# Kernel tuning notes

Hardware: AMD Instinct MI355X
Metric: run time of the kernel (lower is better)

Reference implementation:

```python
import jax, jax.numpy as jnp
import numpy as np

HEADS = 8
DIM_HEAD = 64
DIM = 512
LN_EPS = 1e-5


def rotate_half(t):
    shp = t.shape
    t = t.reshape(*shp[:-1], -1, 2)
    t1, t2 = t[..., 0], t[..., 1]
    return jnp.stack((-t2, t1), axis=-1).reshape(shp)


def apply_rope(freqs, t):
    # freqs: (b,1,n,dh) broadcast against t: (b,h,n,dh); rot_dim == dh so no pass-through
    return t * jnp.cos(freqs) + rotate_half(t) * jnp.sin(freqs)


def layer_norm(x, g, b, eps=LN_EPS):
    mu = jnp.mean(x, axis=-1, keepdims=True)
    var = jnp.var(x, axis=-1, keepdims=True)
    return (x - mu) * jax.lax.rsqrt(var + eps) * g + b


def setup_inputs() -> dict:
    key = jax.random.key(0)
    ks = jax.random.split(key, 8)
    n, b = 2048, 4
    inner = HEADS * DIM_HEAD
    inp = {
        "x": jax.random.normal(ks[0], (n, b, DIM), dtype=jnp.float32),
        "rot_pos_emb": jax.random.uniform(ks[1], (b, n, DIM_HEAD), dtype=jnp.float32),
        "Wq": jax.random.normal(ks[2], (inner, DIM), dtype=jnp.float32) * (DIM ** -0.5),
        "Wk": jax.random.normal(ks[3], (inner, DIM), dtype=jnp.float32) * (DIM ** -0.5),
        "Wv": jax.random.normal(ks[4], (inner, DIM), dtype=jnp.float32) * (DIM ** -0.5),
        "Wo": jax.random.normal(ks[5], (DIM, inner), dtype=jnp.float32) * (inner ** -0.5),
        "bo": jnp.zeros((DIM,), dtype=jnp.float32),
        "ln_g": jnp.ones((DIM,), dtype=jnp.float32),
        "ln_b": jnp.zeros((DIM,), dtype=jnp.float32),
        "head_scale": jnp.ones((1, HEADS, 1, 1), dtype=jnp.float32),
        "ls_scale": jnp.full((1, 1, DIM), 1e-5, dtype=jnp.float32),
    }
    return inp


def reference(x, rot_pos_emb, Wq, Wk, Wv, Wo, bo, ln_g, ln_b, head_scale, ls_scale):
    n, b, d = x.shape
    h, dh = HEADS, DIM_HEAD
    scale = dh ** -0.5

    xb = jnp.transpose(x, (1, 0, 2))  # (b,n,d)
    q = (xb @ Wq.T).reshape(b, n, h, dh).transpose(0, 2, 1, 3)  # (b,h,n,dh)
    k = (xb @ Wk.T).reshape(b, n, h, dh).transpose(0, 2, 1, 3)
    v = (xb @ Wv.T).reshape(b, n, h, dh).transpose(0, 2, 1, 3)

    freqs = rot_pos_emb[:, None]  # (b,1,n,dh)
    q = apply_rope(freqs, q)
    k = apply_rope(freqs, k)

    sim = jnp.einsum("bhid,bhjd->bhij", q, k) * scale
    mask = jnp.triu(jnp.ones((n, n), dtype=bool), 1)
    sim = jnp.where(mask[None, None], -jnp.finfo(sim.dtype).max, sim)
    attn = jax.nn.softmax(sim, axis=-1)

    out = jnp.einsum("bhij,bhjd->bhid", attn, v) * head_scale
    out = out.transpose(0, 2, 1, 3).reshape(b, n, h * dh)
    out = layer_norm(out @ Wo.T + bo, ln_g, ln_b)
    out = jnp.transpose(out, (1, 0, 2))  # (n,b,d)
    return ls_scale * out
```

## Files before the change

### kernel.cpp

```cpp
#include <hip/hip_runtime.h>
#include <hip/hip_bf16.h>
#include <math.h>

#define NSEQ 2048
#define NB 4
#define NH 8
#define DH 64
#define DMODEL 512
#define MROWS (NSEQ * 4)

typedef short bf16x8 __attribute__((ext_vector_type(8)));
typedef float f32x4 __attribute__((ext_vector_type(4)));

static __device__ __forceinline__ short f2bf_r(float f) {
    unsigned u = __float_as_uint(f);
    u += 0x7FFF + ((u >> 16) & 1);
    return (short)(u >> 16);
}
static __device__ __forceinline__ unsigned bfpack(float a, float b) {
    unsigned ua = __float_as_uint(a); ua += 0x7FFF + ((ua >> 16) & 1);
    unsigned ub = __float_as_uint(b); ub += 0x7FFF + ((ub >> 16) & 1);
    return (ua >> 16) | (ub & 0xFFFF0000u);
}
static __device__ __forceinline__ unsigned bfpack_f(float a, float b) {
    unsigned ua = (__float_as_uint(a) + 0x8000u) >> 16;
    unsigned ub = (__float_as_uint(b) + 0x8000u) & 0xFFFF0000u;
    return ua | ub;
}
static __device__ __forceinline__ float bf2f(unsigned short u) {
    return __uint_as_float(((unsigned)u) << 16);
}

__global__ __launch_bounds__(256) void k0_convert(
    const float* __restrict__ x, const float* __restrict__ Wq,
    const float* __restrict__ Wk, const float* __restrict__ Wv,
    const float* __restrict__ Wo, const float* __restrict__ rope,
    __hip_bfloat16* __restrict__ xb, __hip_bfloat16* __restrict__ Wb,
    float* __restrict__ cs, float* __restrict__ sn)
{
    const int idx = blockIdx.x * 256 + threadIdx.x;
    if (idx < 8192 * 128) {
        const int row = idx >> 7, c = (idx & 127) << 2;
        const int bi = row >> 11, ni = row & 2047;
        float4 v = *(const float4*)(x + ((size_t)(ni * NB + bi)) * DMODEL + c);
        uint2 u; u.x = bfpack(v.x, v.y); u.y = bfpack(v.z, v.w);
        *(uint2*)((short*)xb + (size_t)row * 512 + c) = u;
    } else if (idx < 8192 * 128 + 2048 * 128) {
        const int j = idx - 8192 * 128;
        const int row = j >> 7, c = (j & 127) << 2;
        const float* src = (row < 512) ? Wq : (row < 1024) ? Wk
                         : (row < 1536) ? Wv : Wo;
        const int rr = row & 511;
        float4 v = *(const float4*)(src + (size_t)rr * 512 + c);
        uint2 u; u.x = bfpack(v.x, v.y); u.y = bfpack(v.z, v.w);
        *(uint2*)((short*)Wb + (size_t)row * 512 + c) = u;
    } else {
        const int j = idx - (8192 * 128 + 2048 * 128);
        float4 f = *(const float4*)(rope + (size_t)j * 4);
        float4 c4, s4;
        __sincosf(f.x, &s4.x, &c4.x);
        __sincosf(f.y, &s4.y, &c4.y);
        __sincosf(f.z, &s4.z, &c4.z);
        __sincosf(f.w, &s4.w, &c4.w);
        *(float4*)(cs + (size_t)j * 4) = c4;
        *(float4*)(sn + (size_t)j * 4) = s4;
    }
}

__global__ __launch_bounds__(256) void k1_qkv(
    const __hip_bfloat16* __restrict__ xb, const float* __restrict__ cs,
    const float* __restrict__ sn, const __hip_bfloat16* __restrict__ Wb,
    __hip_bfloat16* __restrict__ Qs, __hip_bfloat16* __restrict__ Ks,
    __hip_bfloat16* __restrict__ Vs)
{
    __shared__ short As[128 * 72];
    __shared__ short Bs[128 * 72];
    const int t = threadIdx.x;
    const int w = t >> 6, L = t & 63, lo = L & 15, g = L >> 4;
    const int ah = (w >> 1) << 6;
    const int bhh = (w & 1) << 6;

    const int lid = (int)(blockIdx.y * gridDim.x + blockIdx.x);
    const int xcd = lid & 7, slot = lid >> 3;
    const int row_blk = xcd * 8 + (slot & 7);
    const int col_blk = slot >> 3;
    const int row0 = row_blk * 128, wrow0 = col_blk * 128;
    const int bi = row0 >> 11, ni0 = row0 & 2047;
    const bool isV = (col_blk >= 8);

    f32x4 acc[4][4] = {};
    for (int k0 = 0; k0 < DMODEL; k0 += 64) {
        __syncthreads();
#pragma unroll
        for (int c = 0; c < 4; ++c) {
            const int idx = c * 256 + t;
            const int m = idx >> 3, kb = idx & 7;
            *(uint4*)&As[m * 72 + kb * 8] =
                *(const uint4*)((const short*)xb + (size_t)(row0 + m) * 512 + k0 + kb * 8);
            *(uint4*)&Bs[m * 72 + kb * 8] =
                *(const uint4*)((const short*)Wb + (size_t)(wrow0 + m) * 512 + k0 + kb * 8);
        }
        __syncthreads();
        const short* Abuf = isV ? As : Bs;
        const short* Bbuf = isV ? Bs : As;
#pragma unroll
        for (int ks = 0; ks < 2; ++ks) {
            bf16x8 af[4], bfr[4];
#pragma unroll
            for (int mi = 0; mi < 4; ++mi)
                af[mi] = *(const bf16x8*)&Abuf[(ah + mi * 16 + lo) * 72 + ks * 32 + g * 8];
#pragma unroll
            for (int ni = 0; ni < 4; ++ni)
                bfr[ni] = *(const bf16x8*)&Bbuf[(bhh + ni * 16 + lo) * 72 + ks * 32 + g * 8];
#pragma unroll
            for (int mi = 0; mi < 4; ++mi)
#pragma unroll
                for (int ni = 0; ni < 4; ++ni)
                    acc[mi][ni] = __builtin_amdgcn_mfma_f32_16x16x32_bf16(
                        af[mi], bfr[ni], acc[mi][ni], 0, 0, 0);
        }
    }

    if (!isV) {
        const float SC = 0.125f * 1.44269504088896f;
        short* outp = (short*)((wrow0 < 512) ? Qs : Ks);
        const float qs = (wrow0 < 512) ? SC : 1.0f;
        const int cbase = wrow0 & 511;
#pragma unroll
        for (int mi = 0; mi < 4; ++mi) {
            const int c0 = cbase + ah + mi * 16 + (g << 2);
            const int h = c0 >> 6, e0 = c0 & 63;
            short* hb = outp + ((size_t)(bi * NH + h)) * 131072
                        + (e0 >> 5) * 512 + ((e0 >> 3) & 3) * 128 + (e0 & 7);
#pragma unroll
            for (int ni = 0; ni < 4; ++ni) {
                const int nseq = ni0 + bhh + ni * 16 + lo;
                const float4 c4 = *(const float4*)(cs + ((size_t)bi * NSEQ + nseq) * DH + e0);
                const float4 s4 = *(const float4*)(sn + ((size_t)bi * NSEQ + nseq) * DH + e0);
                const f32x4 v = acc[mi][ni];
                const float o0 = (v[0] * c4.x - v[1] * s4.x) * qs;
                const float o1 = (v[1] * c4.y + v[0] * s4.y) * qs;
                const float o2 = (v[2] * c4.z - v[3] * s4.z) * qs;
                const float o3 = (v[3] * c4.w + v[2] * s4.w) * qs;
                uint2 u; u.x = bfpack(o0, o1); u.y = bfpack(o2, o3);
                *(uint2*)(hb + (size_t)(nseq >> 4) * 1024 + (nseq & 15) * 8) = u;
            }
        }
    } else {
        const int col0 = wrow0 - 1024;
#pragma unroll
        for (int ni = 0; ni < 4; ++ni) {
            const int c = col0 + bhh + ni * 16 + lo;
            const int h = c >> 6, e = c & 63;
            short* hb = (short*)Vs + ((size_t)(bi * NH + h)) * 131072
                        + (e >> 4) * 512 + (e & 15) * 8;
#pragma unroll
            for (int mi = 0; mi < 4; ++mi) {
                const int nb = ni0 + ah + mi * 16 + g * 4;
                uint2 u;
                u.x = bfpack(acc[mi][ni][0], acc[mi][ni][1]);
                u.y = bfpack(acc[mi][ni][2], acc[mi][ni][3]);
                *(uint2*)(hb + (size_t)(nb >> 5) * 2048 + ((nb >> 3) & 3) * 128
                          + (nb & 7)) = u;
            }
        }
    }
}

__global__ __launch_bounds__(256, 3) void k2_attn(
    const __hip_bfloat16* __restrict__ Qs, const __hip_bfloat16* __restrict__ Ks,
    const __hip_bfloat16* __restrict__ Vs, const float* __restrict__ head_scale,
    __hip_bfloat16* __restrict__ Ob)
{
    __shared__ short sP[4][16 * 72];

    const int t = threadIdx.x;
    const int w = t >> 6, L = t & 63, lo = L & 15, g = L >> 4;

    const int lid = (int)blockIdx.x;
    const int xcd = lid & 7, slot = lid >> 3;
    const int bh = xcd * 4 + (slot & 3);
    const int qb = 31 - (slot >> 2);
    const int qt = qb * 4 + w;
    const int bi = bh >> 3, h = bh & 7;

    const short* Kp = (const short*)Ks + (size_t)bh * 131072 + L * 8;
    const short* Qp = (const short*)Qs + (size_t)bh * 131072
                      + (size_t)qt * 1024 + L * 8;
    const bf16x8 qf0 = *(const bf16x8*)(Qp);
    const bf16x8 qf1 = *(const bf16x8*)(Qp + 512);

    f32x4 acc[4] = {};
    float l_i = 0.f;
    const int nkt = qb + 1;

    auto body = [&](const bf16x8* kc0, const bf16x8* kc1,
                    const bf16x8* vb0, const bf16x8* vb1, int kt) {
        const bool diag = (kt == qb);
        const int mlim = diag ? w : 3;
        const bool hi = (mlim >= 2);

        f32x4 s[4];
#pragma unroll
        for (int mt = 0; mt < 4; ++mt) {
            if (mt <= mlim) {
                f32x4 z = {};
                z = __builtin_amdgcn_mfma_f32_16x16x32_bf16(kc0[mt], qf0, z, 0, 0, 0);
                s[mt] = __builtin_amdgcn_mfma_f32_16x16x32_bf16(kc1[mt], qf1, z, 0, 0, 0);
                if (diag && mt == mlim) {
#pragma unroll
                    for (int r = 0; r < 4; ++r)
                        if ((g * 4 + r) > lo) s[mt][r] = -1e30f;
                }
            }
        }

#pragma unroll
        for (int mt = 0; mt < 2; ++mt) {
            uint2 u;
            if (mt <= mlim) {
                const float p0 = exp2f(s[mt][0]);
                const float p1 = exp2f(s[mt][1]);
                const float p2 = exp2f(s[mt][2]);
                const float p3 = exp2f(s[mt][3]);
                l_i += (p0 + p1) + (p2 + p3);
                u.x = bfpack_f(p0, p1); u.y = bfpack_f(p2, p3);
            } else {
                u.x = 0u; u.y = 0u;
            }
            *(uint2*)&sP[w][lo * 72 + mt * 16 + g * 4] = u;
        }
        const bf16x8 pb0 = *(const bf16x8*)&sP[w][lo * 72 + g * 8];
#pragma unroll
        for (int dt = 0; dt < 4; ++dt)
            acc[dt] = __builtin_amdgcn_mfma_f32_16x16x32_bf16(vb0[dt], pb0, acc[dt], 0, 0, 0);

        if (hi) {
#pragma unroll
            for (int mt = 2; mt < 4; ++mt) {
                uint2 u;
                if (mt <= mlim) {
                    const float p0 = exp2f(s[mt][0]);
                    const float p1 = exp2f(s[mt][1]);
                    const float p2 = exp2f(s[mt][2]);
                    const float p3 = exp2f(s[mt][3]);
                    l_i += (p0 + p1) + (p2 + p3);
                    u.x = bfpack_f(p0, p1); u.y = bfpack_f(p2, p3);
                } else {
                    u.x = 0u; u.y = 0u;
                }
                *(uint2*)&sP[w][lo * 72 + mt * 16 + g * 4] = u;
            }
            const bf16x8 pb1 = *(const bf16x8*)&sP[w][lo * 72 + 32 + g * 8];
#pragma unroll
            for (int dt = 0; dt < 4; ++dt)
                acc[dt] = __builtin_amdgcn_mfma_f32_16x16x32_bf16(vb1[dt], pb1, acc[dt], 0, 0, 0);
        }
    };

    bf16x8 kA0[4], kA1[4], kB0[4], kB1[4], vA0[4], vA1[4];
    const short* vp = (const short*)Vs + (size_t)bh * 131072 + L * 8;
    const short* kld = Kp;
#pragma unroll
    for (int mt = 0; mt < 4; ++mt) {
        kA0[mt] = *(const bf16x8*)(kld + mt * 1024);
        kA1[mt] = *(const bf16x8*)(kld + mt * 1024 + 512);
    }
    kld += 4096;
    int kt = 0;
#pragma unroll 1
    while (true) {
        {
            const bool hi = !((kt == qb) && w < 2);
#pragma unroll
            for (int dt = 0; dt < 4; ++dt) {
                vA0[dt] = *(const bf16x8*)(vp + dt * 512);
                if (hi) vA1[dt] = *(const bf16x8*)(vp + (4 + dt) * 512);
            }
        }
        if (kt + 1 < nkt) {
#pragma unroll
            for (int mt = 0; mt < 4; ++mt) {
                kB0[mt] = *(const bf16x8*)(kld + mt * 1024);
                kB1[mt] = *(const bf16x8*)(kld + mt * 1024 + 512);
            }
            kld += 4096;
        }
        body(kA0, kA1, vA0, vA1, kt);
        vp += 4096;
        ++kt;
        if (kt >= nkt) break;

        {
            const bool hi = !((kt == qb) && w < 2);
#pragma unroll
            for (int dt = 0; dt < 4; ++dt) {
                vA0[dt] = *(const bf16x8*)(vp + dt * 512);
                if (hi) vA1[dt] = *(const bf16x8*)(vp + (4 + dt) * 512);
            }
        }
        if (kt + 1 < nkt) {
#pragma unroll
            for (int mt = 0; mt < 4; ++mt) {
                kA0[mt] = *(const bf16x8*)(kld + mt * 1024);
                kA1[mt] = *(const bf16x8*)(kld + mt * 1024 + 512);
            }
            kld += 4096;
        }
        body(kB0, kB1, vA0, vA1, kt);
        vp += 4096;
        ++kt;
        if (kt >= nkt) break;
    }

    l_i += __shfl_xor(l_i, 16);
    l_i += __shfl_xor(l_i, 32);
    const float f = head_scale[h] / l_i;
    const int q = qt * 16 + lo;
    short* op = (short*)Ob + ((size_t)bi * NSEQ + q) * DMODEL + h * DH + g * 4;
#pragma unroll
    for (int dt = 0; dt < 4; ++dt) {
        uint2 u;
        u.x = bfpack(acc[dt][0] * f, acc[dt][1] * f);
        u.y = bfpack(acc[dt][2] * f, acc[dt][3] * f);
        *(uint2*)(op + dt * 16) = u;
    }
}

__global__ __launch_bounds__(256) void k3_proj(
    const __hip_bfloat16* __restrict__ Ob, const __hip_bfloat16* __restrict__ Wob,
    const float* __restrict__ bo, __hip_bfloat16* __restrict__ C2)
{
    __shared__ short As[128 * 72];
    __shared__ short Bs[128 * 72];
    const int t = threadIdx.x;
    const int w = t >> 6, L = t & 63, lo = L & 15, g = L >> 4;
    const int mh = (w >> 1) << 6, nh = (w & 1) << 6;

    const int lid = (int)(blockIdx.y * gridDim.x + blockIdx.x);
    const int xcd = lid & 7, slot = lid >> 3;
    const int row_blk = xcd * 8 + (slot & 7);
    const int col_blk = slot >> 3;
    const int row0 = row_blk * 128, col0 = col_blk * 128;

    f32x4 acc[4][4] = {};
    for (int k0 = 0; k0 < DMODEL; k0 += 64) {
        __syncthreads();
#pragma unroll
        for (int c = 0; c < 4; ++c) {
            const int idx = c * 256 + t;
            const int m = idx >> 3, kb = idx & 7;
            *(uint4*)&As[m * 72 + kb * 8] =
                *(const uint4*)((const short*)Ob + (size_t)(row0 + m) * 512 + k0 + kb * 8);
            *(uint4*)&Bs[m * 72 + kb * 8] =
                *(const uint4*)((const short*)Wob + (size_t)(col0 + m) * 512 + k0 + kb * 8);
        }
        __syncthreads();
#pragma unroll
        for (int ks = 0; ks < 2; ++ks) {
            bf16x8 af[4], bfr[4];
#pragma unroll
            for (int mi = 0; mi < 4; ++mi)
                af[mi] = *(const bf16x8*)&As[(mh + mi * 16 + lo) * 72 + ks * 32 + g * 8];
#pragma unroll
            for (int ni = 0; ni < 4; ++ni)
                bfr[ni] = *(const bf16x8*)&Bs[(nh + ni * 16 + lo) * 72 + ks * 32 + g * 8];
#pragma unroll
            for (int mi = 0; mi < 4; ++mi)
#pragma unroll
                for (int ni = 0; ni < 4; ++ni)
                    acc[mi][ni] = __builtin_amdgcn_mfma_f32_16x16x32_bf16(
                        af[mi], bfr[ni], acc[mi][ni], 0, 0, 0);
        }
    }
#pragma unroll
    for (int ni = 0; ni < 4; ++ni) {
        const int c = col0 + nh + ni * 16 + lo;
        const float b = bo[c];
#pragma unroll
        for (int mi = 0; mi < 4; ++mi) {
#pragma unroll
            for (int r = 0; r < 4; ++r) {
                const int m = row0 + mh + mi * 16 + g * 4 + r;
                *((short*)C2 + (size_t)m * DMODEL + c) = f2bf_r(acc[mi][ni][r] + b);
            }
        }
    }
}

__global__ __launch_bounds__(256) void k4_ln(
    const __hip_bfloat16* __restrict__ C2, const float* __restrict__ g,
    const float* __restrict__ bln, const float* __restrict__ ls,
    float* __restrict__ out)
{
    const int m = blockIdx.x;
    const int bi = m >> 11, ni = m & (NSEQ - 1);
    const unsigned short* row = (const unsigned short*)C2 + (size_t)m * DMODEL;
    const int t = threadIdx.x;
    float v0 = bf2f(row[t]), v1 = bf2f(row[t + 256]);
    float s = v0 + v1, sq2 = v0 * v0 + v1 * v1;
#pragma unroll
    for (int off = 32; off > 0; off >>= 1) {
        s += __shfl_down(s, off);
        sq2 += __shfl_down(sq2, off);
    }
    __shared__ float red[8];
    const int wid = t >> 6;
    if ((t & 63) == 0) { red[wid] = s; red[wid + 4] = sq2; }
    __syncthreads();
    s = red[0] + red[1] + red[2] + red[3];
    sq2 = red[4] + red[5] + red[6] + red[7];
    const float mean = s * (1.f / 512.f);
    const float var = sq2 * (1.f / 512.f) - mean * mean;
    const float rstd = rsqrtf(var + 1e-5f);
    float* ob = out + ((size_t)ni * NB + bi) * DMODEL;
    ob[t]       = ((v0 - mean) * rstd * g[t]       + bln[t])       * ls[t];
    ob[t + 256] = ((v1 - mean) * rstd * g[t + 256] + bln[t + 256]) * ls[t + 256];
}

extern "C" void kernel_launch(void* const* d_in, const int* in_sizes, int n_in,
                              void* d_out, int out_size, void* d_ws, size_t ws_size,
                              hipStream_t stream) {
    const float* x          = (const float*)d_in[0];
    const float* rope       = (const float*)d_in[1];
    const float* Wq         = (const float*)d_in[2];
    const float* Wk         = (const float*)d_in[3];
    const float* Wv         = (const float*)d_in[4];
    const float* Wo         = (const float*)d_in[5];
    const float* bo         = (const float*)d_in[6];
    const float* ln_g       = (const float*)d_in[7];
    const float* ln_b       = (const float*)d_in[8];
    const float* head_scale = (const float*)d_in[9];
    const float* ls_scale   = (const float*)d_in[10];
    float* out = (float*)d_out;

    char* wsb = (char*)d_ws;
    __hip_bfloat16* xb  = (__hip_bfloat16*)(wsb);
    __hip_bfloat16* Wb  = (__hip_bfloat16*)(wsb + ((size_t) 8 << 20));
    __hip_bfloat16* Qs  = (__hip_bfloat16*)(wsb + ((size_t)10 << 20));
    __hip_bfloat16* Ks  = (__hip_bfloat16*)(wsb + ((size_t)18 << 20));
    __hip_bfloat16* Vs  = (__hip_bfloat16*)(wsb + ((size_t)26 << 20));
    __hip_bfloat16* Ob  = (__hip_bfloat16*)(wsb + ((size_t)34 << 20));
    float*          cs  = (float*)(wsb + ((size_t)42 << 20));
    float*          sn  = (float*)(wsb + ((size_t)44 << 20));
    __hip_bfloat16* C2  = (__hip_bfloat16*)(wsb + ((size_t)10 << 20));
    __hip_bfloat16* Wob = Wb + (size_t)1536 * 512;

    k0_convert<<<5632, 256, 0, stream>>>(x, Wq, Wk, Wv, Wo, rope, xb, Wb, cs, sn);
    k1_qkv<<<dim3(64, 12), 256, 0, stream>>>(xb, cs, sn, Wb, Qs, Ks, Vs);
    k2_attn<<<1024, 256, 0, stream>>>(Qs, Ks, Vs, head_scale, Ob);
    k3_proj<<<dim3(64, 4), 256, 0, stream>>>(Ob, Wob, bo, C2);
    k4_ln<<<MROWS, 256, 0, stream>>>(C2, ln_g, ln_b, ls_scale, out);
}
```

Baseline: 177.0 us.

## Fuse x bf16 conversion into QKV GEMM and split attention into single-wave blocks

The standalone x-to-bf16 conversion pass is removed; the QKV GEMM now reads fp32 x directly, with the transpose folded into its addressing, and packs to bf16 while staging into shared memory. This saves a full write and re-read of the converted activations. Attention blocks shrink from four waves to one wave per 16-query tile, launched as four times as many blocks, with per-block causal limits so waves no longer wait on their slowest sibling. The cost is double the fp32 global read traffic in the GEMM, and K/V tiles that were shared across four waves in L2 are now fetched by separate blocks.

```diff
diff --git a/kernel.cpp b/kernel.cpp
--- a/kernel.cpp
+++ b/kernel.cpp
@@ -32,22 +32,15 @@
 }
 
 __global__ __launch_bounds__(256) void k0_convert(
-    const float* __restrict__ x, const float* __restrict__ Wq,
-    const float* __restrict__ Wk, const float* __restrict__ Wv,
-    const float* __restrict__ Wo, const float* __restrict__ rope,
-    __hip_bfloat16* __restrict__ xb, __hip_bfloat16* __restrict__ Wb,
-    float* __restrict__ cs, float* __restrict__ sn)
+    const float* __restrict__ Wq, const float* __restrict__ Wk,
+    const float* __restrict__ Wv, const float* __restrict__ Wo,
+    const float* __restrict__ rope,
+    __hip_bfloat16* __restrict__ Wb, float* __restrict__ cs,
+    float* __restrict__ sn)
 {
     const int idx = blockIdx.x * 256 + threadIdx.x;
-    if (idx < 8192 * 128) {
+    if (idx < 2048 * 128) {
         const int row = idx >> 7, c = (idx & 127) << 2;
-        const int bi = row >> 11, ni = row & 2047;
-        float4 v = *(const float4*)(x + ((size_t)(ni * NB + bi)) * DMODEL + c);
-        uint2 u; u.x = bfpack(v.x, v.y); u.y = bfpack(v.z, v.w);
-        *(uint2*)((short*)xb + (size_t)row * 512 + c) = u;
-    } else if (idx < 8192 * 128 + 2048 * 128) {
-        const int j = idx - 8192 * 128;
-        const int row = j >> 7, c = (j & 127) << 2;
         const float* src = (row < 512) ? Wq : (row < 1024) ? Wk
                          : (row < 1536) ? Wv : Wo;
         const int rr = row & 511;
@@ -55,7 +48,7 @@
         uint2 u; u.x = bfpack(v.x, v.y); u.y = bfpack(v.z, v.w);
         *(uint2*)((short*)Wb + (size_t)row * 512 + c) = u;
     } else {
-        const int j = idx - (8192 * 128 + 2048 * 128);
+        const int j = idx - 2048 * 128;
         float4 f = *(const float4*)(rope + (size_t)j * 4);
         float4 c4, s4;
         __sincosf(f.x, &s4.x, &c4.x);
@@ -68,7 +61,7 @@
 }
 
 __global__ __launch_bounds__(256) void k1_qkv(
-    const __hip_bfloat16* __restrict__ xb, const float* __restrict__ cs,
+    const float* __restrict__ x, const float* __restrict__ cs,
     const float* __restrict__ sn, const __hip_bfloat16* __restrict__ Wb,
     __hip_bfloat16* __restrict__ Qs, __hip_bfloat16* __restrict__ Ks,
     __hip_bfloat16* __restrict__ Vs)
@@ -95,8 +88,12 @@
         for (int c = 0; c < 4; ++c) {
             const int idx = c * 256 + t;
             const int m = idx >> 3, kb = idx & 7;
-            *(uint4*)&As[m * 72 + kb * 8] =
-                *(const uint4*)((const short*)xb + (size_t)(row0 + m) * 512 + k0 + kb * 8);
+            const float* xp = x + ((size_t)((ni0 + m) * NB + bi)) * DMODEL + k0 + kb * 8;
+            float4 xv0 = *(const float4*)(xp);
+            float4 xv1 = *(const float4*)(xp + 4);
+            uint4 xu = { bfpack(xv0.x, xv0.y), bfpack(xv0.z, xv0.w),
+                         bfpack(xv1.x, xv1.y), bfpack(xv1.z, xv1.w) };
+            *(uint4*)&As[m * 72 + kb * 8] = xu;
             *(uint4*)&Bs[m * 72 + kb * 8] =
                 *(const uint4*)((const short*)Wb + (size_t)(wrow0 + m) * 512 + k0 + kb * 8);
         }
@@ -167,22 +164,22 @@
     }
 }
 
-__global__ __launch_bounds__(256, 3) void k2_attn(
+__global__ __launch_bounds__(64, 6) void k2_attn(
     const __hip_bfloat16* __restrict__ Qs, const __hip_bfloat16* __restrict__ Ks,
     const __hip_bfloat16* __restrict__ Vs, const float* __restrict__ head_scale,
     __hip_bfloat16* __restrict__ Ob)
 {
-    __shared__ short sP[4][16 * 72];
-
-    const int t = threadIdx.x;
-    const int w = t >> 6, L = t & 63, lo = L & 15, g = L >> 4;
+    __shared__ short sP[16 * 72];
+
+    const int L = threadIdx.x;
+    const int lo = L & 15, g = L >> 4;
 
     const int lid = (int)blockIdx.x;
     const int xcd = lid & 7, slot = lid >> 3;
     const int bh = xcd * 4 + (slot & 3);
-    const int qb = 31 - (slot >> 2);
-    const int qt = qb * 4 + w;
+    const int qt = 127 - (slot >> 2);
     const int bi = bh >> 3, h = bh & 7;
+    const int qm = qt & 3;
 
     const short* Kp = (const short*)Ks + (size_t)bh * 131072 + L * 8;
     const short* Qp = (const short*)Qs + (size_t)bh * 131072
@@ -192,12 +189,12 @@
 
     f32x4 acc[4] = {};
     float l_i = 0.f;
-    const int nkt = qb + 1;
+    const int nkt = (qt >> 2) + 1;
 
     auto body = [&](const bf16x8* kc0, const bf16x8* kc1,
                     const bf16x8* vb0, const bf16x8* vb1, int kt) {
-        const bool diag = (kt == qb);
-        const int mlim = diag ? w : 3;
+        const bool diag = (kt == nkt - 1);
+        const int mlim = diag ? qm : 3;
         const bool hi = (mlim >= 2);
 
         f32x4 s[4];
@@ -228,9 +225,9 @@
             } else {
                 u.x = 0u; u.y = 0u;
             }
-            *(uint2*)&sP[w][lo * 72 + mt * 16 + g * 4] = u;
-        }
-        const bf16x8 pb0 = *(const bf16x8*)&sP[w][lo * 72 + g * 8];
+            *(uint2*)&sP[lo * 72 + mt * 16 + g * 4] = u;
+        }
+        const bf16x8 pb0 = *(const bf16x8*)&sP[lo * 72 + g * 8];
 #pragma unroll
         for (int dt = 0; dt < 4; ++dt)
             acc[dt] = __builtin_amdgcn_mfma_f32_16x16x32_bf16(vb0[dt], pb0, acc[dt], 0, 0, 0);
@@ -249,9 +246,9 @@
                 } else {
                     u.x = 0u; u.y = 0u;
                 }
-                *(uint2*)&sP[w][lo * 72 + mt * 16 + g * 4] = u;
-            }
-            const bf16x8 pb1 = *(const bf16x8*)&sP[w][lo * 72 + 32 + g * 8];
+                *(uint2*)&sP[lo * 72 + mt * 16 + g * 4] = u;
+            }
+            const bf16x8 pb1 = *(const bf16x8*)&sP[lo * 72 + 32 + g * 8];
 #pragma unroll
             for (int dt = 0; dt < 4; ++dt)
                 acc[dt] = __builtin_amdgcn_mfma_f32_16x16x32_bf16(vb1[dt], pb1, acc[dt], 0, 0, 0);
@@ -271,11 +268,11 @@
 #pragma unroll 1
     while (true) {
         {
-            const bool hi = !((kt == qb) && w < 2);
+            const bool hiv = !((kt == nkt - 1) && qm < 2);
 #pragma unroll
             for (int dt = 0; dt < 4; ++dt) {
                 vA0[dt] = *(const bf16x8*)(vp + dt * 512);
-                if (hi) vA1[dt] = *(const bf16x8*)(vp + (4 + dt) * 512);
+                if (hiv) vA1[dt] = *(const bf16x8*)(vp + (4 + dt) * 512);
             }
         }
         if (kt + 1 < nkt) {
@@ -292,11 +289,11 @@
         if (kt >= nkt) break;
 
         {
-            const bool hi = !((kt == qb) && w < 2);
+            const bool hiv = !((kt == nkt - 1) && qm < 2);
 #pragma unroll
             for (int dt = 0; dt < 4; ++dt) {
                 vA0[dt] = *(const bf16x8*)(vp + dt * 512);
-                if (hi) vA1[dt] = *(const bf16x8*)(vp + (4 + dt) * 512);
+                if (hiv) vA1[dt] = *(const bf16x8*)(vp + (4 + dt) * 512);
             }
         }
         if (kt + 1 < nkt) {
@@ -435,20 +432,19 @@
     float* out = (float*)d_out;
 
     char* wsb = (char*)d_ws;
-    __hip_bfloat16* xb  = (__hip_bfloat16*)(wsb);
-    __hip_bfloat16* Wb  = (__hip_bfloat16*)(wsb + ((size_t) 8 << 20));
-    __hip_bfloat16* Qs  = (__hip_bfloat16*)(wsb + ((size_t)10 << 20));
-    __hip_bfloat16* Ks  = (__hip_bfloat16*)(wsb + ((size_t)18 << 20));
-    __hip_bfloat16* Vs  = (__hip_bfloat16*)(wsb + ((size_t)26 << 20));
-    __hip_bfloat16* Ob  = (__hip_bfloat16*)(wsb + ((size_t)34 << 20));
-    float*          cs  = (float*)(wsb + ((size_t)42 << 20));
-    float*          sn  = (float*)(wsb + ((size_t)44 << 20));
-    __hip_bfloat16* C2  = (__hip_bfloat16*)(wsb + ((size_t)10 << 20));
+    __hip_bfloat16* Wb  = (__hip_bfloat16*)(wsb);
+    __hip_bfloat16* Qs  = (__hip_bfloat16*)(wsb + ((size_t) 2 << 20));
+    __hip_bfloat16* Ks  = (__hip_bfloat16*)(wsb + ((size_t)10 << 20));
+    __hip_bfloat16* Vs  = (__hip_bfloat16*)(wsb + ((size_t)18 << 20));
+    __hip_bfloat16* Ob  = (__hip_bfloat16*)(wsb + ((size_t)26 << 20));
+    float*          cs  = (float*)(wsb + ((size_t)34 << 20));
+    float*          sn  = (float*)(wsb + ((size_t)36 << 20));
+    __hip_bfloat16* C2  = Qs;
     __hip_bfloat16* Wob = Wb + (size_t)1536 * 512;
 
-    k0_convert<<<5632, 256, 0, stream>>>(x, Wq, Wk, Wv, Wo, rope, xb, Wb, cs, sn);
-    k1_qkv<<<dim3(64, 12), 256, 0, stream>>>(xb, cs, sn, Wb, Qs, Ks, Vs);
-    k2_attn<<<1024, 256, 0, stream>>>(Qs, Ks, Vs, head_scale, Ob);
+    k0_convert<<<1536, 256, 0, stream>>>(Wq, Wk, Wv, Wo, rope, Wb, cs, sn);
+    k1_qkv<<<dim3(64, 12), 256, 0, stream>>>(x, cs, sn, Wb, Qs, Ks, Vs);
+    k2_attn<<<4096, 64, 0, stream>>>(Qs, Ks, Vs, head_scale, Ob);
     k3_proj<<<dim3(64, 4), 256, 0, stream>>>(Ob, Wob, bo, C2);
     k4_ln<<<MROWS, 256, 0, stream>>>(C2, ln_g, ln_b, ls_scale, out);
 }
```

Result: slower. 360.8 us (+103.9%).
